# Kernel tuning notes

Measured on AMD Instinct MI355X. Metric: run time of the kernel, lower is better.

## Reference

```python
import jax, jax.numpy as jnp
import numpy as np

D_MODEL = 2048
N_HEADS = 16
N_KV = 4
D_HEAD = D_MODEL // N_HEADS  # 128
KERNEL = 4
TOTAL_QKV = (N_HEADS + 2 * N_KV) * D_HEAD  # 3072
BATCH, SEQ = 2, 2048


def setup_inputs() -> dict:
    key = jax.random.key(0)
    ks = jax.random.split(key, 6)
    s = 1.0 / np.sqrt(D_MODEL)
    return {
        "hidden_states": jax.random.normal(ks[0], (BATCH, SEQ, D_MODEL), jnp.float32),
        "w_q": jax.random.normal(ks[1], (D_MODEL, N_HEADS * D_HEAD), jnp.float32) * s,
        "w_k": jax.random.normal(ks[2], (D_MODEL, N_KV * D_HEAD), jnp.float32) * s,
        "w_v": jax.random.normal(ks[3], (D_MODEL, N_KV * D_HEAD), jnp.float32) * s,
        "w_o": jax.random.normal(ks[4], (N_HEADS * D_HEAD, D_MODEL), jnp.float32) * s,
        "conv_w": jax.random.normal(ks[5], (TOTAL_QKV, KERNEL), jnp.float32) * 0.1,
    }


def _canon_b(x, conv_w):
    """Depthwise causal conv1d with residual. x: [B,S,C], conv_w: [C,K]."""
    K = conv_w.shape[1]
    xp = jnp.pad(x, ((0, 0), (K - 1, 0), (0, 0)))  # left pad for causality
    S = x.shape[1]
    out = sum(xp[:, k:k + S, :] * conv_w[:, k] for k in range(K))
    return x + out


def reference(hidden_states, w_q, w_k, w_v, w_o, conv_w):
    B, S, _ = hidden_states.shape
    q = hidden_states @ w_q   # [B,S,Hq*Dh]
    k = hidden_states @ w_k   # [B,S,Hkv*Dh]
    v = hidden_states @ w_v
    qkv = jnp.concatenate([q, k, v], axis=-1)
    qkv = _canon_b(qkv, conv_w)
    q_dim = N_HEADS * D_HEAD
    kv_dim = N_KV * D_HEAD
    q, k, v = jnp.split(qkv, [q_dim, q_dim + kv_dim], axis=-1)
    q = q.reshape(B, S, N_HEADS, D_HEAD)
    k = k.reshape(B, S, N_KV, D_HEAD)
    v = v.reshape(B, S, N_KV, D_HEAD)
    # GQA: repeat kv heads to match query heads
    groups = N_HEADS // N_KV
    k = jnp.repeat(k, groups, axis=2)
    v = jnp.repeat(v, groups, axis=2)
    scale = 1.0 / np.sqrt(D_HEAD)
    scores = jnp.einsum("bqhd,bkhd->bhqk", q, k) * scale  # [B,H,S,S]
    causal = jnp.tril(jnp.ones((S, S), dtype=bool))
    scores = jnp.where(causal, scores, jnp.finfo(scores.dtype).min)
    probs = jax.nn.softmax(scores, axis=-1)
    attended = jnp.einsum("bhqk,bkhd->bqhd", probs, v)  # [B,S,H,Dh]
    attended = attended.reshape(B, S, N_HEADS * D_HEAD)
    return attended @ w_o
```

## Files before the change

kernel.cpp:

```cpp
#include <hip/hip_runtime.h>
#include <stdint.h>

typedef unsigned short u16;
typedef short short8 __attribute__((ext_vector_type(8)));
typedef float f32x4 __attribute__((ext_vector_type(4)));
typedef float f32x16 __attribute__((ext_vector_type(16)));

#define DM    2048
#define NH    16
#define NKV   4
#define DH    128
#define TQKV  3072
#define NB    2
#define SEQL  2048
#define MROWS (NB * SEQL)
#define QDIM  (NH * DH)
#define KVDIM (NKV * DH)
#define QSCALE_L2E 0.1275174336f

#define MFMA16(a, b, c) __builtin_amdgcn_mfma_f32_16x16x32_bf16((a), (b), (c), 0, 0, 0)
#define MFMA32(a, b, c) __builtin_amdgcn_mfma_f32_32x32x16_bf16((a), (b), (c), 0, 0, 0)

__device__ __forceinline__ u16 f2bf(float f) {
  uint32_t u = __float_as_uint(f);
  u += 0x7fffu + ((u >> 16) & 1u);
  return (u16)(u >> 16);
}
__device__ __forceinline__ float bf2f(u16 h) {
  return __uint_as_float(((uint32_t)h) << 16);
}
__device__ __forceinline__ void gload16(const u16* g, u16* l) {
  __builtin_amdgcn_global_load_lds((__attribute__((address_space(1))) void*)(u16*)g,
                                   (__attribute__((address_space(3))) void*)l, 16, 0, 0);
}
__device__ __forceinline__ uint32_t cvtpk(float lo, float hi) {
  uint32_t r;
  asm("v_cvt_pk_bf16_f32 %0, %1, %2" : "=v"(r) : "v"(lo), "v"(hi));
  return r;
}
__device__ __forceinline__ void swapln(uint32_t& a, uint32_t& b) {
  asm volatile("v_permlane32_swap_b32 %0, %1" : "+v"(a), "+v"(b));
}

__global__ __launch_bounds__(256) void k_prep(const float* __restrict__ hin,
                                              const float* __restrict__ wq,
                                              const float* __restrict__ wk,
                                              const float* __restrict__ wvv,
                                              const float* __restrict__ wo,
                                              u16* __restrict__ h_bf,
                                              u16* __restrict__ Wt,
                                              u16* __restrict__ Wot) {
  __shared__ float t[32][33];
  const int bid = blockIdx.x;
  const int tid = threadIdx.x;
  if (bid < 8192) {
    const int i = (bid * 256 + tid) * 4;
    float4 v = *reinterpret_cast<const float4*>(hin + i);
    u16* d = h_bf + i;
    d[0] = f2bf(v.x); d[1] = f2bf(v.y); d[2] = f2bf(v.z); d[3] = f2bf(v.w);
    return;
  }
  const float* src; u16* dst; int N, rowOff, bx, by;
  if (bid < 12288)      { const int r = bid - 8192;  src = wq;  dst = Wt;  N = 2048; rowOff = 0;    bx = r & 63; by = r >> 6; }
  else if (bid < 13312) { const int r = bid - 12288; src = wk;  dst = Wt;  N = 512;  rowOff = 2048; bx = r & 15; by = r >> 4; }
  else if (bid < 14336) { const int r = bid - 13312; src = wvv; dst = Wt;  N = 512;  rowOff = 2560; bx = r & 15; by = r >> 4; }
  else                  { const int r = bid - 14336; src = wo;  dst = Wot; N = 2048; rowOff = 0;    bx = r & 63; by = r >> 6; }
  const int n0 = bx * 32, k0 = by * 32;
  const int tx = tid & 31, ty = tid >> 5;
#pragma unroll
  for (int i = ty; i < 32; i += 8)
    t[i][tx] = src[(size_t)(k0 + i) * N + (n0 + tx)];
  __syncthreads();
#pragma unroll
  for (int i = ty; i < 32; i += 8)
    dst[(size_t)(rowOff + n0 + i) * 2048 + (k0 + tx)] = f2bf(t[tx][i]);
}

__global__ void k_transpose_bf16(const u16* __restrict__ src, u16* __restrict__ dst, int R, int C) {
  __shared__ u16 t[32][33];
  const size_t zoff = (size_t)blockIdx.z * R * C;
  const int c0 = blockIdx.x * 32, r0 = blockIdx.y * 32;
  const int tx = threadIdx.x, ty = threadIdx.y;
#pragma unroll
  for (int i = ty; i < 32; i += 8)
    t[i][tx] = src[zoff + (size_t)(r0 + i) * C + (c0 + tx)];
  __syncthreads();
#pragma unroll
  for (int i = ty; i < 32; i += 8)
    dst[zoff + (size_t)(c0 + i) * R + (r0 + tx)] = t[tx][i];
}

template <int OUTBF>
__global__ __launch_bounds__(256) void k_gemm_bt(const u16* __restrict__ A, const u16* __restrict__ Bt,
                                                 float* __restrict__ Cf, u16* __restrict__ Cb,
                                                 int M, int N, int K) {
  __shared__ u16 As[2][128 * 32];
  __shared__ u16 Bs[2][128 * 32];
  const int tid = threadIdx.x;
  const int m0 = blockIdx.x * 128;
  const int n0 = blockIdx.y * 128;
  const int r  = tid >> 2;
  const int c8 = (tid & 3) << 3;
  const u16* Ag0 = A  + (size_t)(m0 + r) * K + c8;
  const u16* Ag1 = A  + (size_t)(m0 + 64 + r) * K + c8;
  const u16* Bg0 = Bt + (size_t)(n0 + r) * K + c8;
  const u16* Bg1 = Bt + (size_t)(n0 + 64 + r) * K + c8;

  auto stage = [&](int buf, int kt) {
    const int kg = kt * 32;
    gload16(Ag0 + kg, &As[buf][tid * 8]);
    gload16(Ag1 + kg, &As[buf][2048 + tid * 8]);
    gload16(Bg0 + kg, &Bs[buf][tid * 8]);
    gload16(Bg1 + kg, &Bs[buf][2048 + tid * 8]);
  };

  f32x4 acc[4][4];
#pragma unroll
  for (int i = 0; i < 4; ++i)
#pragma unroll
    for (int j = 0; j < 4; ++j) acc[i][j] = (f32x4){0.f, 0.f, 0.f, 0.f};

  const int wv = tid >> 6, ln = tid & 63;
  const int wr = (wv >> 1) * 64, wc = (wv & 1) * 64;
  const int lr = ln & 15, lko = (ln >> 4) * 8;

  stage(0, 0);
  __syncthreads();

  const int nk = K >> 5;
  for (int kt = 0; kt < nk; ++kt) {
    const int cur = kt & 1;
    if (kt + 1 < nk) stage(cur ^ 1, kt + 1);
    short8 af[4], bf[4];
#pragma unroll
    for (int i = 0; i < 4; ++i)
      af[i] = *reinterpret_cast<const short8*>(&As[cur][(wr + i * 16 + lr) * 32 + lko]);
#pragma unroll
    for (int i = 0; i < 4; ++i)
      bf[i] = *reinterpret_cast<const short8*>(&Bs[cur][(wc + i * 16 + lr) * 32 + lko]);
#pragma unroll
    for (int i = 0; i < 4; ++i)
#pragma unroll
      for (int j = 0; j < 4; ++j)
        acc[i][j] = MFMA16(af[i], bf[j], acc[i][j]);
    __syncthreads();
  }

  const int rg = (ln >> 4) * 4;
#pragma unroll
  for (int i = 0; i < 4; ++i) {
#pragma unroll
    for (int j = 0; j < 4; ++j) {
      const int row = m0 + wr + i * 16 + rg;
      const int col = n0 + wc + j * 16 + lr;
#pragma unroll
      for (int q = 0; q < 4; ++q) {
        float v = acc[i][j][q];
        if (OUTBF) Cb[(size_t)(row + q) * N + col] = f2bf(v);
        else       Cf[(size_t)(row + q) * N + col] = v;
      }
    }
  }
}

__global__ void k_conv_route(const u16* __restrict__ qkv, const float* __restrict__ cw,
                             u16* __restrict__ Qh, u16* __restrict__ Kh, u16* __restrict__ Vsd) {
  const int row = blockIdx.x;
  const int b = row >> 11, s = row & 2047;
  const int c = threadIdx.x * 8;
  float x[4][8];
#pragma unroll
  for (int k = 0; k < 4; ++k) {
    const int sr = s + k - 3;
    if (sr < 0) {
#pragma unroll
      for (int j = 0; j < 8; ++j) x[k][j] = 0.f;
    } else {
      short8 v = *reinterpret_cast<const short8*>(&qkv[(size_t)(b * SEQL + sr) * TQKV + c]);
#pragma unroll
      for (int j = 0; j < 8; ++j) x[k][j] = bf2f((u16)v[j]);
    }
  }
  float o[8];
#pragma unroll
  for (int j = 0; j < 8; ++j) {
    float4 w4 = *reinterpret_cast<const float4*>(&cw[(c + j) * 4]);
    o[j] = x[3][j] + x[0][j] * w4.x + x[1][j] * w4.y + x[2][j] * w4.z + x[3][j] * w4.w;
  }
  short8 ov;
  if (c < QDIM) {
#pragma unroll
    for (int j = 0; j < 8; ++j) ov[j] = (short)f2bf(o[j] * QSCALE_L2E);
    const int h = c >> 7, d = c & 127;
    *reinterpret_cast<short8*>(&Qh[((size_t)(b * NH + h) * SEQL + s) * DH + d]) = ov;
  } else if (c < QDIM + KVDIM) {
#pragma unroll
    for (int j = 0; j < 8; ++j) ov[j] = (short)f2bf(o[j]);
    const int cc = c - QDIM;
    const int h = cc >> 7, d = cc & 127;
    *reinterpret_cast<short8*>(&Kh[((size_t)(b * NKV + h) * SEQL + s) * DH + d]) = ov;
  } else {
#pragma unroll
    for (int j = 0; j < 8; ++j) ov[j] = (short)f2bf(o[j]);
    const int cc = c - QDIM - KVDIM;
    const int h = cc >> 7, d = cc & 127;
    *reinterpret_cast<short8*>(&Vsd[((size_t)(b * NKV + h) * SEQL + s) * DH + d]) = ov;
  }
}

__global__ __launch_bounds__(512) void k_attn(const u16* __restrict__ Qh, const u16* __restrict__ Kh,
                                              const u16* __restrict__ Vt, u16* __restrict__ att,
                                              u16* __restrict__ pO, float* __restrict__ pm,
                                              float* __restrict__ pl) {
  static const int qbA_t[8] = {7,6,5,4,7,6,5,4};
  static const int tA0_t[8] = {0,0,0,0,18,18,18,18};
  static const int tA1_t[8] = {18,18,18,18,32,28,24,20};
  static const int chkA_t[8]= {0,0,0,0,1,1,1,1};
  static const int qbB_t[8] = {0,0,0,0,0,1,2,3};
  static const int tB1_t[8] = {0,0,0,0,4,8,12,16};

  const int slot = blockIdx.x >> 5;
  const int bh = blockIdx.x & 31;
  const int s = bh & 7, tt = bh >> 3;
  const int b = s >> 2, kvh = s & 3;
  const int h = kvh * 4 + tt;
  const int bhl = b * NH + h;

  __shared__ u16 Ks[3][64 * 128];
  __shared__ u16 Vs[3][128 * 64];
  const int tid = threadIdx.x, wv = tid >> 6, ln = tid & 63;
  const int lq = ln & 31, hi = ln >> 5;
  const int hi16 = hi * 16;
  const int swk = (lq & 15) << 4;

  const u16* kg = Kh + (size_t)(b * NKV + kvh) * SEQL * DH;
  const u16* vg = Vt + (size_t)(b * NKV + kvh) * DH * SEQL;

  const int ck0 = tid, ck1 = tid + 512;
  const int krow0 = ck0 >> 4, kcb0 = (ck0 & 15) << 4;
  const int krow1 = ck1 >> 4, kcb1 = (ck1 & 15) << 4;
  const int koff0 = krow0 * DH + ((kcb0 ^ ((krow0 & 15) << 4)) >> 1);
  const int koff1 = krow1 * DH + ((kcb1 ^ ((krow1 & 15) << 4)) >> 1);
  const int vline0 = ck0 >> 4, vslotG0 = (ck0 & 15) ^ (vline0 & 15);
  const int vline1 = ck1 >> 4, vslotG1 = (ck1 & 15) ^ (vline1 & 15);
  const int voff0 = (vline0 * 2 + (vslotG0 >> 3)) * SEQL + (vslotG0 & 7) * 8;
  const int voff1 = (vline1 * 2 + (vslotG1 >> 3)) * SEQL + (vslotG1 & 7) * 8;

  auto stage = [&](int buf, int kvs) {
    gload16(kg + (size_t)kvs * DH + koff0, &Ks[buf][ck0 * 8]);
    gload16(kg + (size_t)kvs * DH + koff1, &Ks[buf][ck1 * 8]);
    gload16(vg + (size_t)kvs + voff0, &Vs[buf][ck0 * 8]);
    gload16(vg + (size_t)kvs + voff1, &Vs[buf][ck1 * 8]);
  };

  for (int seg = 0; seg < 2; ++seg) {
    int qb, tA, tB, split, chk;
    if (seg == 0) {
      qb = qbA_t[slot]; tA = tA0_t[slot]; tB = tA1_t[slot]; split = 1; chk = chkA_t[slot];
    } else {
      tB = tB1_t[slot];
      if (tB == 0) break;
      qb = qbB_t[slot]; tA = 0; split = 0; chk = 0;
    }

    const int q0w = qb * 256 + wv * 32;
    const int qg = q0w + lq;

    const u16* qrow = Qh + ((size_t)(b * NH + h) * SEQL + qg) * DH;
    short8 qf[8];
#pragma unroll
    for (int dblk = 0; dblk < 8; ++dblk)
      qf[dblk] = *reinterpret_cast<const short8*>(qrow + dblk * 16 + hi * 8);

    f32x16 oacc[4];
#pragma unroll
    for (int nb = 0; nb < 4; ++nb)
#pragma unroll
      for (int rq = 0; rq < 16; ++rq) oacc[nb][rq] = 0.f;
    float mrow = -1e30f, lrow = 0.f;

    stage(0, tA * 64);
    if (tA + 1 < tB) stage(1, (tA + 1) * 64);
    int cur = 0;

    for (int t = tA; t < tB; ++t) {
      if (t + 1 < tB) { asm volatile("s_waitcnt vmcnt(4)" ::: "memory"); }
      else            { asm volatile("s_waitcnt vmcnt(0)" ::: "memory"); }
      __builtin_amdgcn_s_barrier();
      const int nxt = (cur == 2) ? 0 : cur + 1;
      const int nn  = (nxt == 2) ? 0 : nxt + 1;
      if (t + 2 < tB) stage(nn, (t + 2) * 64);
      const int kvs = t * 64;
      if (kvs <= q0w + 31) {
        const u16* ks = Ks[cur];
        const u16* vs = Vs[cur];
        f32x16 st[2];
#pragma unroll
        for (int kvb = 0; kvb < 2; ++kvb)
#pragma unroll
          for (int rq = 0; rq < 16; ++rq) st[kvb][rq] = 0.f;

        __builtin_amdgcn_s_setprio(1);
#pragma unroll
        for (int kvb = 0; kvb < 2; ++kvb) {
          const u16* krow = ks + (kvb * 32 + lq) * 128;
#pragma unroll
          for (int dblk = 0; dblk < 8; ++dblk) {
            short8 kf = *reinterpret_cast<const short8*>(krow + (((dblk * 32 + hi16) ^ swk) >> 1));
            st[kvb] = MFMA32(kf, qf[dblk], st[kvb]);
          }
        }
        __builtin_amdgcn_s_setprio(0);

        if (kvs + 63 > q0w) {
#pragma unroll
          for (int kvb = 0; kvb < 2; ++kvb)
#pragma unroll
            for (int rq = 0; rq < 16; ++rq) {
              const int kvg = kvs + kvb * 32 + (rq & 3) + 8 * (rq >> 2) + 4 * hi;
              if (kvg > qg) st[kvb][rq] = -1e30f;
            }
        }

        float a0 = st[0][0], a1 = st[0][1], a2 = st[0][2], a3 = st[0][3];
#pragma unroll
        for (int kvb = 0; kvb < 2; ++kvb)
#pragma unroll
          for (int rq = (kvb ? 0 : 4); rq < 16; rq += 4) {
            a0 = fmaxf(a0, st[kvb][rq]);
            a1 = fmaxf(a1, st[kvb][rq + 1]);
            a2 = fmaxf(a2, st[kvb][rq + 2]);
            a3 = fmaxf(a3, st[kvb][rq + 3]);
          }
        float tm = fmaxf(fmaxf(a0, a1), fmaxf(a2, a3));
        tm = fmaxf(tm, __shfl_xor(tm, 32));
        if (__any(tm > mrow + 11.0f)) {
          const float nm = fmaxf(mrow, tm);
          const float scl = exp2f(mrow - nm);
          mrow = nm;
          lrow *= scl;
#pragma unroll
          for (int nb = 0; nb < 4; ++nb)
#pragma unroll
            for (int rq = 0; rq < 16; ++rq) oacc[nb][rq] *= scl;
        }
        float s0 = 0.f, s1 = 0.f, s2 = 0.f, s3 = 0.f;
#pragma unroll
        for (int kvb = 0; kvb < 2; ++kvb)
#pragma unroll
          for (int rq = 0; rq < 16; rq += 4) {
            float p0 = exp2f(st[kvb][rq] - mrow);
            float p1 = exp2f(st[kvb][rq + 1] - mrow);
            float p2 = exp2f(st[kvb][rq + 2] - mrow);
            float p3 = exp2f(st[kvb][rq + 3] - mrow);
            st[kvb][rq] = p0; st[kvb][rq + 1] = p1; st[kvb][rq + 2] = p2; st[kvb][rq + 3] = p3;
            s0 += p0; s1 += p1; s2 += p2; s3 += p3;
          }
        float ps = (s0 + s1) + (s2 + s3);
        ps += __shfl_xor(ps, 32);
        lrow += ps;

        uint32_t w[4][4];
#pragma unroll
        for (int kvb = 0; kvb < 2; ++kvb) {
          uint32_t x0 = cvtpk(st[kvb][0], st[kvb][1]);
          uint32_t y0 = cvtpk(st[kvb][4], st[kvb][5]);
          swapln(x0, y0);
          uint32_t x1 = cvtpk(st[kvb][2], st[kvb][3]);
          uint32_t y1 = cvtpk(st[kvb][6], st[kvb][7]);
          swapln(x1, y1);
          w[kvb * 2][0] = x0; w[kvb * 2][1] = x1; w[kvb * 2][2] = y0; w[kvb * 2][3] = y1;
          uint32_t x2 = cvtpk(st[kvb][8], st[kvb][9]);
          uint32_t y2 = cvtpk(st[kvb][12], st[kvb][13]);
          swapln(x2, y2);
          uint32_t x3 = cvtpk(st[kvb][10], st[kvb][11]);
          uint32_t y3 = cvtpk(st[kvb][14], st[kvb][15]);
          swapln(x3, y3);
          w[kvb * 2 + 1][0] = x2; w[kvb * 2 + 1][1] = x3; w[kvb * 2 + 1][2] = y2; w[kvb * 2 + 1][3] = y3;
        }
        short8 pa[4];
#pragma unroll
        for (int kc = 0; kc < 4; ++kc) {
          union { uint32_t uw[4]; short8 s; } pu;
#pragma unroll
          for (int j = 0; j < 4; ++j) pu.uw[j] = w[kc][j];
          pa[kc] = pu.s;
        }

        __builtin_amdgcn_s_setprio(1);
        const int vsw = lq >> 1;
        const int sbase = (lq & 1) << 3;
#pragma unroll
        for (int nb = 0; nb < 4; ++nb) {
          const u16* vline = vs + (nb * 16 + (lq >> 1)) * 128;
#pragma unroll
          for (int kc = 0; kc < 4; ++kc) {
            short8 vf = *reinterpret_cast<const short8*>(vline + (((sbase | (kc * 2 + hi)) ^ vsw) << 3));
            oacc[nb] = MFMA32(vf, pa[kc], oacc[nb]);
          }
        }
        __builtin_amdgcn_s_setprio(0);
      }
      cur = nxt;
    }

    if (!split) {
      const float inv = 1.0f / lrow;
      u16* orow = att + ((size_t)(b * SEQL + qg)) * QDIM + h * DH;
#pragma unroll
      for (int nb = 0; nb < 4; ++nb)
#pragma unroll
        for (int rg = 0; rg < 4; ++rg) {
          const int rq = rg * 4;
          uint2 vout;
          vout.x = cvtpk(oacc[nb][rq] * inv, oacc[nb][rq + 1] * inv);
          vout.y = cvtpk(oacc[nb][rq + 2] * inv, oacc[nb][rq + 3] * inv);
          *reinterpret_cast<uint2*>(orow + nb * 32 + 8 * rg + 4 * hi) = vout;
        }
    } else {
      const int rowp = ((bhl * 4 + (qb - 4)) << 8) + wv * 32 + lq;
      u16* prow = pO + (size_t)chk * 32768 * 128 + (size_t)rowp * 128;
#pragma unroll
      for (int nb = 0; nb < 4; ++nb)
#pragma unroll
        for (int rg = 0; rg < 4; ++rg) {
          const int rq = rg * 4;
          uint2 vout;
          vout.x = cvtpk(oacc[nb][rq], oacc[nb][rq + 1]);
          vout.y = cvtpk(oacc[nb][rq + 2], oacc[nb][rq + 3]);
          *reinterpret_cast<uint2*>(prow + nb * 32 + 8 * rg + 4 * hi) = vout;
        }
      if (!hi) {
        pm[chk * 32768 + rowp] = mrow;
        pl[chk * 32768 + rowp] = lrow;
      }
    }
    __syncthreads();
  }
}

__global__ void k_combine(const u16* __restrict__ pO, const float* __restrict__ pm,
                          const float* __restrict__ pl, u16* __restrict__ att) {
  const int e = blockIdx.x * 256 + threadIdx.x;
  const int rowp = e >> 4;
  const int d8 = (e & 15) * 8;
  const float m0 = pm[rowp], m1 = pm[32768 + rowp];
  const float l0 = pl[rowp], l1 = pl[32768 + rowp];
  const float mm = fmaxf(m0, m1);
  const float a0 = exp2f(m0 - mm), a1 = exp2f(m1 - mm);
  const float inv = 1.0f / (l0 * a0 + l1 * a1);
  const float w0 = a0 * inv, w1 = a1 * inv;
  short8 o0 = *reinterpret_cast<const short8*>(pO + (size_t)rowp * 128 + d8);
  short8 o1 = *reinterpret_cast<const short8*>(pO + (size_t)32768 * 128 + (size_t)rowp * 128 + d8);
  const int bh = rowp >> 10, qb = 4 + ((rowp >> 8) & 3), r = rowp & 255;
  const int b = bh >> 4, h = bh & 15;
  u16* orow = att + ((size_t)(b * SEQL + qb * 256 + r)) * QDIM + h * DH + d8;
  uint2 vout;
  float r0 = bf2f((u16)o0[0]) * w0 + bf2f((u16)o1[0]) * w1;
  float r1 = bf2f((u16)o0[1]) * w0 + bf2f((u16)o1[1]) * w1;
  float r2 = bf2f((u16)o0[2]) * w0 + bf2f((u16)o1[2]) * w1;
  float r3 = bf2f((u16)o0[3]) * w0 + bf2f((u16)o1[3]) * w1;
  float r4 = bf2f((u16)o0[4]) * w0 + bf2f((u16)o1[4]) * w1;
  float r5 = bf2f((u16)o0[5]) * w0 + bf2f((u16)o1[5]) * w1;
  float r6 = bf2f((u16)o0[6]) * w0 + bf2f((u16)o1[6]) * w1;
  float r7 = bf2f((u16)o0[7]) * w0 + bf2f((u16)o1[7]) * w1;
  vout.x = ((uint32_t)f2bf(r1) << 16) | f2bf(r0);
  vout.y = ((uint32_t)f2bf(r3) << 16) | f2bf(r2);
  uint2 vout2;
  vout2.x = ((uint32_t)f2bf(r5) << 16) | f2bf(r4);
  vout2.y = ((uint32_t)f2bf(r7) << 16) | f2bf(r6);
  *reinterpret_cast<uint2*>(orow) = vout;
  *reinterpret_cast<uint2*>(orow + 4) = vout2;
}

extern "C" void kernel_launch(void* const* d_in, const int* in_sizes, int n_in,
                              void* d_out, int out_size, void* d_ws, size_t ws_size,
                              hipStream_t stream) {
  const float* hin = (const float*)d_in[0];
  const float* wq  = (const float*)d_in[1];
  const float* wk  = (const float*)d_in[2];
  const float* wvv = (const float*)d_in[3];
  const float* wo  = (const float*)d_in[4];
  const float* cw  = (const float*)d_in[5];
  float* out = (float*)d_out;
  char* ws = (char*)d_ws;

  u16* h_bf = (u16*)(ws + 0);
  u16* Wt   = (u16*)(ws + 16777216);
  u16* Wot  = (u16*)(ws + 29360128);
  u16* Qh   = (u16*)(ws + 37748736);
  u16* Kh   = (u16*)(ws + 54525952);
  u16* Vsd  = (u16*)(ws + 58720256);
  u16* Vt   = (u16*)(ws + 62914560);
  u16* att  = (u16*)(ws + 67108864);
  u16* qkv  = (u16*)d_out;
  u16*   pO = (u16*)d_out;
  float* pm = (float*)((char*)d_out + 16777216);
  float* pl = (float*)((char*)d_out + 16777216 + 262144);

  dim3 tb(32, 8);
  k_prep<<<dim3(18432), 256, 0, stream>>>(hin, wq, wk, wvv, wo, h_bf, Wt, Wot);
  k_gemm_bt<1><<<dim3(32, 24), 256, 0, stream>>>(h_bf, Wt, nullptr, qkv, MROWS, TQKV, DM);
  k_conv_route<<<MROWS, 384, 0, stream>>>(qkv, cw, Qh, Kh, Vsd);
  k_transpose_bf16<<<dim3(4, 64, NB * NKV), tb, 0, stream>>>(Vsd, Vt, SEQL, DH);
  k_attn<<<dim3(256), 512, 0, stream>>>(Qh, Kh, Vt, att, pO, pm, pl);
  k_combine<<<dim3(2048), 256, 0, stream>>>(pO, pm, pl, att);
  k_gemm_bt<0><<<dim3(32, 16), 256, 0, stream>>>(att, Wot, out, nullptr, MROWS, DM, DM);
}
```

Before: 226.3 us.

## Replace QKV projection GEMM with 256x256-tile 8-wave pingpong kernel

Adds a new GEMM kernel with 256x256 output tiles, 8 waves, 64-deep K steps, XOR-swizzled LDS staging via direct global-to-LDS loads, and barrier-interleaved phases with s_setprio around MFMA bursts. It is used for the QKV projection in place of the 128x128 kernel. The aim is more data reuse per LDS byte and better overlap of loads with MFMA work. The cost is a grid of only 192 blocks on a 256-CU device and 128 KB of LDS per block, which limits occupancy. The output projection still uses the old kernel.

```diff
diff --git a/kernel.cpp b/kernel.cpp
--- a/kernel.cpp
+++ b/kernel.cpp
@@ -88,6 +88,141 @@
 #pragma unroll
   for (int i = ty; i < 32; i += 8)
     dst[zoff + (size_t)(c0 + i) * R + (r0 + tx)] = t[tx][i];
+}
+
+template <int OUTBF>
+__global__ __launch_bounds__(512) void k_gemm8p(const u16* __restrict__ A, const u16* __restrict__ Bt,
+                                                float* __restrict__ Cf, u16* __restrict__ Cb,
+                                                int M, int N, int K) {
+  __shared__ u16 lds[65536];
+  const int tid = threadIdx.x;
+  const int m0 = blockIdx.x * 256, n0 = blockIdx.y * 256;
+  const int wv = tid >> 6, ln = tid & 63;
+  const int wm = wv >> 2, wn = wv & 3;
+  const int lr = ln & 15, lg4 = ln >> 4, lr7 = lr & 7;
+
+  const int sr0 = tid >> 3,         ss0 = ((tid & 7) ^ (sr0 & 7)) * 8;
+  const int sr1 = (tid + 512) >> 3, ss1 = (((tid + 512) & 7) ^ (sr1 & 7)) * 8;
+
+  auto stage = [&](int buf, int kt) {
+#pragma unroll
+    for (int mat = 0; mat < 2; ++mat) {
+      const u16* gs = mat ? Bt : A;
+      const int rb = mat ? n0 : m0;
+#pragma unroll
+      for (int hf = 0; hf < 2; ++hf) {
+        u16* dst = &lds[((buf * 2 + mat) * 2 + hf) * 8192];
+        gload16(gs + (size_t)(rb + hf * 128 + sr0) * K + kt * 64 + ss0, dst + tid * 8);
+        gload16(gs + (size_t)(rb + hf * 128 + sr1) * K + kt * 64 + ss1, dst + (tid + 512) * 8);
+      }
+    }
+  };
+
+  f32x4 acc[8][4];
+#pragma unroll
+  for (int i = 0; i < 8; ++i)
+#pragma unroll
+    for (int j = 0; j < 4; ++j) acc[i][j] = (f32x4){0.f, 0.f, 0.f, 0.f};
+
+  const int nk = K >> 6;
+  stage(0, 0);
+
+  const int bro = (wn & 1) * 64;
+  for (int t = 0; t < nk; ++t) {
+    const int buf = t & 1;
+    const u16* Ah = &lds[((buf * 2 + 0) * 2 + wm) * 8192];
+    const u16* Bh = &lds[((buf * 2 + 1) * 2 + (wn >> 1)) * 8192];
+    short8 af[4][2], bf[2][2], bg[2][2];
+
+    asm volatile("s_waitcnt vmcnt(0)" ::: "memory");
+    __builtin_amdgcn_s_barrier();
+    if (t + 1 < nk) stage(buf ^ 1, t + 1);
+#pragma unroll
+    for (int i = 0; i < 4; ++i)
+#pragma unroll
+      for (int kk = 0; kk < 2; ++kk)
+        af[i][kk] = *reinterpret_cast<const short8*>(
+            &Ah[(i * 16 + lr) * 64 + (((kk * 4 + lg4) ^ lr7)) * 8]);
+#pragma unroll
+    for (int j = 0; j < 2; ++j)
+#pragma unroll
+      for (int kk = 0; kk < 2; ++kk)
+        bf[j][kk] = *reinterpret_cast<const short8*>(
+            &Bh[(bro + j * 16 + lr) * 64 + (((kk * 4 + lg4) ^ lr7)) * 8]);
+    __builtin_amdgcn_s_setprio(1);
+#pragma unroll
+    for (int i = 0; i < 4; ++i)
+#pragma unroll
+      for (int j = 0; j < 2; ++j)
+#pragma unroll
+        for (int kk = 0; kk < 2; ++kk)
+          acc[i][j] = MFMA16(af[i][kk], bf[j][kk], acc[i][j]);
+    __builtin_amdgcn_s_setprio(0);
+    __builtin_amdgcn_s_barrier();
+
+#pragma unroll
+    for (int j = 0; j < 2; ++j)
+#pragma unroll
+      for (int kk = 0; kk < 2; ++kk)
+        bg[j][kk] = *reinterpret_cast<const short8*>(
+            &Bh[(bro + (2 + j) * 16 + lr) * 64 + (((kk * 4 + lg4) ^ lr7)) * 8]);
+    __builtin_amdgcn_s_barrier();
+    __builtin_amdgcn_s_setprio(1);
+#pragma unroll
+    for (int i = 0; i < 4; ++i)
+#pragma unroll
+      for (int j = 0; j < 2; ++j)
+#pragma unroll
+        for (int kk = 0; kk < 2; ++kk)
+          acc[i][2 + j] = MFMA16(af[i][kk], bg[j][kk], acc[i][2 + j]);
+    __builtin_amdgcn_s_setprio(0);
+    __builtin_amdgcn_s_barrier();
+
+#pragma unroll
+    for (int i = 0; i < 4; ++i)
+#pragma unroll
+      for (int kk = 0; kk < 2; ++kk)
+        af[i][kk] = *reinterpret_cast<const short8*>(
+            &Ah[((4 + i) * 16 + lr) * 64 + (((kk * 4 + lg4) ^ lr7)) * 8]);
+    __builtin_amdgcn_s_barrier();
+    __builtin_amdgcn_s_setprio(1);
+#pragma unroll
+    for (int i = 0; i < 4; ++i)
+#pragma unroll
+      for (int j = 0; j < 2; ++j)
+#pragma unroll
+        for (int kk = 0; kk < 2; ++kk)
+          acc[4 + i][j] = MFMA16(af[i][kk], bf[j][kk], acc[4 + i][j]);
+    __builtin_amdgcn_s_setprio(0);
+    __builtin_amdgcn_s_barrier();
+
+    __builtin_amdgcn_s_barrier();
+    __builtin_amdgcn_s_setprio(1);
+#pragma unroll
+    for (int i = 0; i < 4; ++i)
+#pragma unroll
+      for (int j = 0; j < 2; ++j)
+#pragma unroll
+        for (int kk = 0; kk < 2; ++kk)
+          acc[4 + i][2 + j] = MFMA16(af[i][kk], bg[j][kk], acc[4 + i][2 + j]);
+    __builtin_amdgcn_s_setprio(0);
+    __builtin_amdgcn_s_barrier();
+  }
+
+  const int rg = lg4 * 4;
+#pragma unroll
+  for (int i = 0; i < 8; ++i)
+#pragma unroll
+    for (int j = 0; j < 4; ++j) {
+      const int row = m0 + wm * 128 + i * 16 + rg;
+      const int col = n0 + wn * 64 + j * 16 + lr;
+#pragma unroll
+      for (int q = 0; q < 4; ++q) {
+        float v = acc[i][j][q];
+        if (OUTBF) Cb[(size_t)(row + q) * N + col] = f2bf(v);
+        else       Cf[(size_t)(row + q) * N + col] = v;
+      }
+    }
 }
 
 template <int OUTBF>
@@ -500,7 +635,7 @@
 
   dim3 tb(32, 8);
   k_prep<<<dim3(18432), 256, 0, stream>>>(hin, wq, wk, wvv, wo, h_bf, Wt, Wot);
-  k_gemm_bt<1><<<dim3(32, 24), 256, 0, stream>>>(h_bf, Wt, nullptr, qkv, MROWS, TQKV, DM);
+  k_gemm8p<1><<<dim3(16, 12), 512, 0, stream>>>(h_bf, Wt, nullptr, qkv, MROWS, TQKV, DM);
   k_conv_route<<<MROWS, 384, 0, stream>>>(qkv, cw, Qh, Kh, Vsd);
   k_transpose_bf16<<<dim3(4, 64, NB * NKV), tb, 0, stream>>>(Vsd, Vt, SEQL, DH);
   k_attn<<<dim3(256), 512, 0, stream>>>(Qh, Kh, Vt, att, pO, pm, pl);
```

Measured after the change: 227.0 us. Within noise of the previous version (+0.3%).
